# Kernel tuning notes

Hardware: AMD Instinct MI355X
Metric: run time of the kernel (lower is better)

## Reference

```python
import jax, jax.numpy as jnp
import numpy as np

B = 8
N1, N2 = 65536, 16384
C1, C2 = 256, 512
BN_EPS = 1e-5


def setup_inputs() -> dict:
    key = jax.random.key(0)
    ks = jax.random.split(key, 8)
    xyz1 = jax.random.normal(ks[0], (N1, 3), dtype=jnp.float32)
    points1 = jax.random.normal(ks[1], (N1, C1), dtype=jnp.float32)
    xyz2 = jax.random.normal(ks[2], (N2, 3), dtype=jnp.float32)
    points2 = jax.random.normal(ks[3], (N2, C2), dtype=jnp.float32)
    offset1 = (jnp.arange(1, B + 1, dtype=jnp.int32) * (N1 // B))
    offset2 = (jnp.arange(1, B + 1, dtype=jnp.int32) * (N2 // B))
    W1 = jax.random.normal(ks[4], (C1 + C2, 256), dtype=jnp.float32) * 0.02
    b1 = jnp.zeros((256,), jnp.float32)
    g1 = jnp.ones((256,), jnp.float32)
    be1 = jnp.zeros((256,), jnp.float32)
    W2 = jax.random.normal(ks[5], (256, 256), dtype=jnp.float32) * 0.02
    b2 = jnp.zeros((256,), jnp.float32)
    g2 = jnp.ones((256,), jnp.float32)
    be2 = jnp.zeros((256,), jnp.float32)
    return dict(xyz1=xyz1, points1=points1, xyz2=xyz2, points2=points2,
                offset1=offset1, offset2=offset2,
                W1=W1, b1=b1, g1=g1, be1=be1, W2=W2, b2=b2, g2=g2, be2=be2)


def _knn3(q, k):
    # q: [n1,3] queries, k: [n2,3] reference set -> 3-NN idx + euclidean dist
    d2 = (jnp.sum(q * q, -1)[:, None] + jnp.sum(k * k, -1)[None, :]
          - 2.0 * (q @ k.T))                      # [n1, n2]
    neg_d2, idx = jax.lax.top_k(-d2, 3)           # [n1, 3]
    dist = jnp.sqrt(jnp.maximum(-neg_d2, 0.0))
    return idx, dist


def _bn_relu(x, g, be):
    # BatchNorm1d in training mode: biased batch stats over the point dim
    mu = jnp.mean(x, axis=0)
    var = jnp.mean((x - mu) ** 2, axis=0)
    return jax.nn.relu(g * (x - mu) * jax.lax.rsqrt(var + BN_EPS) + be)


def reference(xyz1, points1, xyz2, points2, offset1, offset2,
              W1, b1, g1, be1, W2, b2, g2, be2):
    bsz = offset1.shape[0]
    n1 = xyz1.shape[0] // bsz
    n2 = xyz2.shape[0] // bsz
    q = xyz1.reshape(bsz, n1, 3)
    k = xyz2.reshape(bsz, n2, 3)
    idx, dist = jax.vmap(_knn3)(q, k)             # [B,n1,3], [B,n1,3]
    gidx = (idx + (jnp.arange(bsz, dtype=idx.dtype) * n2)[:, None, None])
    gidx = gidx.reshape(-1, 3)                    # [N1,3] global row ids
    dist = dist.reshape(-1, 3)
    dist_recip = 1.0 / (dist + 1e-8)
    weight = dist_recip / jnp.sum(dist_recip, axis=1, keepdims=True)
    # fused gather + weighted accumulate: [N1,3,C2] * [N1,3,1] -> [N1,C2]
    interpolated = jnp.sum(points2[gidx] * weight[..., None], axis=1)
    x = jnp.concatenate([points1, interpolated], axis=1)  # [N1, C1+C2]
    x = _bn_relu(x @ W1 + b1, g1, be1)
    x = _bn_relu(x @ W2 + b2, g2, be2)
    return x
```

## Files before the change

### kernel.cpp

```cpp
#include <hip/hip_runtime.h>
#include <math.h>

#define N1T 65536
#define N2T 16384
#define BSZ 8
#define N1B 8192
#define N2B 2048
#define C1 256
#define C2 512
#define K1 768
#define HID 256
#define BN_EPS 1e-5f

typedef short bf16x8 __attribute__((ext_vector_type(8)));
typedef float f32x4 __attribute__((ext_vector_type(4)));

__device__ __forceinline__ float mul_rn(float a, float b) {
    float r; asm("v_mul_f32 %0, %1, %2" : "=v"(r) : "v"(a), "v"(b)); return r;
}
__device__ __forceinline__ float add_rn(float a, float b) {
    float r; asm("v_add_f32 %0, %1, %2" : "=v"(r) : "v"(a), "v"(b)); return r;
}
__device__ __forceinline__ float sub_rn(float a, float b) {
    float r; asm("v_sub_f32 %0, %1, %2" : "=v"(r) : "v"(a), "v"(b)); return r;
}
__device__ __forceinline__ float fma_rn(float a, float b, float c) {
    float r; asm("v_fma_f32 %0, %1, %2, %3" : "=v"(r) : "v"(a), "v"(b), "v"(c)); return r;
}
__device__ __forceinline__ short f2bf(float f) {
    unsigned u = __builtin_bit_cast(unsigned, f);
    u += 0x7fffu + ((u >> 16) & 1u);
    return (short)(u >> 16);
}
__device__ __forceinline__ float bf2f(short s) {
    return __builtin_bit_cast(float, ((unsigned)(unsigned short)s) << 16);
}

__global__ __launch_bounds__(256) void knn_kernel(
    const float* __restrict__ xyz1, const float* __restrict__ xyz2,
    int* __restrict__ idx_out, float* __restrict__ w_out)
{
    __shared__ float4 sref[N2B + 4];
    const int tid = threadIdx.x;
    const int qbase = blockIdx.x * 64;
    const int batch = qbase / N1B;
    const float* k2 = xyz2 + (size_t)batch * N2B * 3;
    for (int p = tid; p < N2B; p += 256) {
        float x = k2[3 * p], y = k2[3 * p + 1], z = k2[3 * p + 2];
        float kk = add_rn(add_rn(mul_rn(x, x), mul_rn(y, y)), mul_rn(z, z));
        sref[p + (p >> 9)] = make_float4(x, y, z, kk);
    }
    __syncthreads();

    const int q = qbase + (tid >> 2);
    const int sub = tid & 3;
    const float qx = xyz1[q * 3 + 0], qy = xyz1[q * 3 + 1], qz = xyz1[q * 3 + 2];
    const float qq = add_rn(add_rn(mul_rn(qx, qx), mul_rn(qy, qy)), mul_rn(qz, qz));

    const int base = sub * 513;
    const int gbase = sub * 512;
    float a0 = 1e30f, a1 = 1e30f, a2 = 1e30f;
    int   ai0 = 0x7fffffff, ai1 = 0x7fffffff, ai2 = 0x7fffffff;
    float c0 = 1e30f, c1 = 1e30f, c2 = 1e30f;
    int   ci0 = 0x7fffffff, ci1 = 0x7fffffff, ci2 = 0x7fffffff;
    for (int jj = 0; jj < 256; ++jj) {
        float4 rA = sref[base + jj];
        float4 rB = sref[base + 256 + jj];
        float pA = mul_rn(qx, rA.x);
        float tA = fma_rn(qz, rA.z, fma_rn(qy, rA.y, pA));
        float dA = add_rn(sub_rn(qq, add_rn(tA, tA)), rA.w);
        float pB = mul_rn(qx, rB.x);
        float tB = fma_rn(qz, rB.z, fma_rn(qy, rB.y, pB));
        float dB = add_rn(sub_rn(qq, add_rn(tB, tB)), rB.w);
        if (dA < a2) {
            if (dA < a1) {
                a2 = a1; ai2 = ai1;
                if (dA < a0) { a1 = a0; ai1 = ai0; a0 = dA; ai0 = gbase + jj; }
                else         { a1 = dA; ai1 = gbase + jj; }
            } else { a2 = dA; ai2 = gbase + jj; }
        }
        if (dB < c2) {
            if (dB < c1) {
                c2 = c1; ci2 = ci1;
                if (dB < c0) { c1 = c0; ci1 = ci0; c0 = dB; ci0 = gbase + 256 + jj; }
                else         { c1 = dB; ci1 = gbase + 256 + jj; }
            } else { c2 = dB; ci2 = gbase + 256 + jj; }
        }
    }
    float bd0 = a0, bd1 = a1, bd2 = a2;
    int   bi0 = ai0, bi1 = ai1, bi2 = ai2;
#define LEXINS(d, ji)                                                        \
    if ((d < bd2) || (d == bd2 && ji < bi2)) {                               \
        if ((d < bd1) || (d == bd1 && ji < bi1)) {                           \
            bd2 = bd1; bi2 = bi1;                                            \
            if ((d < bd0) || (d == bd0 && ji < bi0)) {                       \
                bd1 = bd0; bi1 = bi0; bd0 = d; bi0 = ji;                     \
            } else { bd1 = d; bi1 = ji; }                                    \
        } else { bd2 = d; bi2 = ji; }                                        \
    }
    LEXINS(c0, ci0) LEXINS(c1, ci1) LEXINS(c2, ci2)
#pragma unroll
    for (int mask = 1; mask <= 2; mask <<= 1) {
        float pd0 = __shfl_xor(bd0, mask, 64);
        float pd1 = __shfl_xor(bd1, mask, 64);
        float pd2 = __shfl_xor(bd2, mask, 64);
        int   pi0 = __shfl_xor(bi0, mask, 64);
        int   pi1 = __shfl_xor(bi1, mask, 64);
        int   pi2 = __shfl_xor(bi2, mask, 64);
        LEXINS(pd0, pi0) LEXINS(pd1, pi1) LEXINS(pd2, pi2)
    }
#undef LEXINS
    if (sub == 0) {
        float d0s = __fsqrt_rn(fmaxf(bd0, 0.0f));
        float d1s = __fsqrt_rn(fmaxf(bd1, 0.0f));
        float d2s = __fsqrt_rn(fmaxf(bd2, 0.0f));
        float r0 = __fdiv_rn(1.0f, add_rn(d0s, 1e-8f));
        float r1 = __fdiv_rn(1.0f, add_rn(d1s, 1e-8f));
        float r2 = __fdiv_rn(1.0f, add_rn(d2s, 1e-8f));
        float rs = add_rn(add_rn(r0, r1), r2);
        w_out[q * 3 + 0] = __fdiv_rn(r0, rs);
        w_out[q * 3 + 1] = __fdiv_rn(r1, rs);
        w_out[q * 3 + 2] = __fdiv_rn(r2, rs);
        idx_out[q * 3 + 0] = batch * N2B + bi0;
        idx_out[q * 3 + 1] = batch * N2B + bi1;
        idx_out[q * 3 + 2] = batch * N2B + bi2;
    }
}

__global__ __launch_bounds__(256) void cast_p2_kernel(
    const float* __restrict__ p2, short* __restrict__ p2b)
{
    const size_t i = ((size_t)blockIdx.x * 256 + threadIdx.x) * 8;
    float4 u0 = *(const float4*)(p2 + i);
    float4 u1 = *(const float4*)(p2 + i + 4);
    bf16x8 v;
    v[0] = f2bf(u0.x); v[1] = f2bf(u0.y); v[2] = f2bf(u0.z); v[3] = f2bf(u0.w);
    v[4] = f2bf(u1.x); v[5] = f2bf(u1.y); v[6] = f2bf(u1.z); v[7] = f2bf(u1.w);
    *(bf16x8*)(p2b + i) = v;
}

__global__ __launch_bounds__(256) void transpose_w_kernel(
    const float* __restrict__ Win, short* __restrict__ WT, int K, int N)
{
    const int e = blockIdx.x * 256 + threadIdx.x;
    const int k = e / N, n = e % N;
    WT[(size_t)n * K + k] = f2bf(Win[e]);
}

#define LDP 40

__global__ __launch_bounds__(512) void gemm1m_kernel(
    const float* __restrict__ points1, const short* __restrict__ p2b,
    const int* __restrict__ idx, const float* __restrict__ w,
    const short* __restrict__ w1t, const float* __restrict__ bias,
    short* __restrict__ y1b, float* __restrict__ psum, float* __restrict__ psq)
{
    __shared__ short As[128][LDP];
    __shared__ short Bs[256][LDP];
    __shared__ float redS[2][4][64], redQ[2][4][64];
    const int tid = threadIdx.x;
    const int lane = tid & 63, wv = tid >> 6;
    const int wr = wv >> 2, wc = wv & 3;
    const int l16 = lane & 15, kh = (lane >> 4) * 8;
    const int row0 = blockIdx.x * 128;
    f32x4 acc[4][4];
#pragma unroll
    for (int m = 0; m < 4; ++m)
#pragma unroll
        for (int n = 0; n < 4; ++n) acc[m][n] = (f32x4){0.f, 0.f, 0.f, 0.f};

    const int arow = tid >> 2, akc = (tid & 3) * 8;
    const int rowA = row0 + arow;
    const int   jA0 = idx[rowA * 3 + 0], jA1 = idx[rowA * 3 + 1], jA2 = idx[rowA * 3 + 2];
    const float wA0 = w[rowA * 3 + 0],   wA1 = w[rowA * 3 + 1],   wA2 = w[rowA * 3 + 2];
    const int cb0 = tid * 2, cb1 = tid * 2 + 1;
    const int brow0 = cb0 >> 2, bkc0 = (cb0 & 3) * 8;
    const int brow1 = cb1 >> 2, bkc1 = (cb1 & 3) * 8;

#define LOAD_A(VA, KT)                                                        \
    {                                                                         \
        const int k0_ = (KT) * 32;                                            \
        if (k0_ < C1) {                                                       \
            float4 u0 = *(const float4*)(points1 + (size_t)rowA * C1 + k0_ + akc);     \
            float4 u1 = *(const float4*)(points1 + (size_t)rowA * C1 + k0_ + akc + 4); \
            VA[0] = f2bf(u0.x); VA[1] = f2bf(u0.y); VA[2] = f2bf(u0.z); VA[3] = f2bf(u0.w); \
            VA[4] = f2bf(u1.x); VA[5] = f2bf(u1.y); VA[6] = f2bf(u1.z); VA[7] = f2bf(u1.w); \
        } else {                                                              \
            const int kb = k0_ - C1 + akc;                                    \
            bf16x8 ga = *(const bf16x8*)(p2b + (size_t)jA0 * C2 + kb);        \
            bf16x8 gb = *(const bf16x8*)(p2b + (size_t)jA1 * C2 + kb);        \
            bf16x8 gc = *(const bf16x8*)(p2b + (size_t)jA2 * C2 + kb);        \
            _Pragma("unroll")                                                 \
            for (int e = 0; e < 8; ++e)                                       \
                VA[e] = f2bf(fmaf(bf2f(ga[e]), wA0,                           \
                          fmaf(bf2f(gb[e]), wA1, bf2f(gc[e]) * wA2)));        \
        }                                                                     \
    }
#define LOAD_B(WA, WB, KT)                                                    \
    {                                                                         \
        const int k0_ = (KT) * 32;                                            \
        WA = *(const bf16x8*)(w1t + (size_t)brow0 * K1 + k0_ + bkc0);         \
        WB = *(const bf16x8*)(w1t + (size_t)brow1 * K1 + k0_ + bkc1);         \
    }

    bf16x8 va, wa, wb;
    LOAD_A(va, 0)
    LOAD_B(wa, wb, 0)
    for (int kt = 0; kt < K1 / 32; ++kt) {
        __syncthreads();
        *(bf16x8*)(&As[arow][akc]) = va;
        *(bf16x8*)(&Bs[brow0][bkc0]) = wa;
        *(bf16x8*)(&Bs[brow1][bkc1]) = wb;
        __syncthreads();
        if (kt + 1 < K1 / 32) {
            LOAD_A(va, kt + 1)
            LOAD_B(wa, wb, kt + 1)
        }
        bf16x8 af[4], bf[4];
#pragma unroll
        for (int m = 0; m < 4; ++m)
            af[m] = *(const bf16x8*)(&As[wr * 64 + m * 16 + l16][kh]);
#pragma unroll
        for (int n = 0; n < 4; ++n)
            bf[n] = *(const bf16x8*)(&Bs[wc * 64 + n * 16 + l16][kh]);
#pragma unroll
        for (int m = 0; m < 4; ++m)
#pragma unroll
            for (int n = 0; n < 4; ++n)
                acc[m][n] = __builtin_amdgcn_mfma_f32_16x16x32_bf16(
                    af[m], bf[n], acc[m][n], 0, 0, 0);
    }
#undef LOAD_A
#undef LOAD_B
#pragma unroll
    for (int n = 0; n < 4; ++n) {
        const int col = wc * 64 + n * 16 + l16;
        const float bv = bias[col];
        float s = 0.f, qa = 0.f;
#pragma unroll
        for (int m = 0; m < 4; ++m) {
            const int rowb = row0 + wr * 64 + m * 16 + (lane >> 4) * 4;
#pragma unroll
            for (int j = 0; j < 4; ++j) {
                float v = acc[m][n][j] + bv;
                y1b[(size_t)(rowb + j) * HID + col] = f2bf(v);
                s += v; qa = fmaf(v, v, qa);
            }
        }
        s += __shfl_xor(s, 16, 64);  s += __shfl_xor(s, 32, 64);
        qa += __shfl_xor(qa, 16, 64); qa += __shfl_xor(qa, 32, 64);
        if ((lane >> 4) == 0) {
            redS[wr][wc][n * 16 + l16] = s;
            redQ[wr][wc][n * 16 + l16] = qa;
        }
    }
    __syncthreads();
    if (tid < 256) {
        const int wcf = tid >> 6, cf = tid & 63;
        float s = redS[0][wcf][cf] + redS[1][wcf][cf];
        float qa = redQ[0][wcf][cf] + redQ[1][wcf][cf];
        psum[(size_t)blockIdx.x * HID + tid] = s;
        psq[(size_t)blockIdx.x * HID + tid] = qa;
    }
}

#define GEMM_EPILOGUE(STORE_STMT)                                             \
    __shared__ float redS[2][2][64], redQ[2][2][64];                          \
    _Pragma("unroll")                                                         \
    for (int n = 0; n < 4; ++n) {                                             \
        const int col = col0 + wc * 64 + n * 16 + l16;                        \
        const float bv = bias[col];                                           \
        float s = 0.f, qa = 0.f;                                              \
        _Pragma("unroll")                                                     \
        for (int m = 0; m < 4; ++m) {                                         \
            const int rowb = row0 + wr * 64 + m * 16 + (lane >> 4) * 4;       \
            _Pragma("unroll")                                                 \
            for (int j = 0; j < 4; ++j) {                                     \
                float v = acc[m][n][j] + bv;                                  \
                STORE_STMT;                                                   \
                s += v; qa = fmaf(v, v, qa);                                  \
            }                                                                 \
        }                                                                     \
        s += __shfl_xor(s, 16, 64);  s += __shfl_xor(s, 32, 64);              \
        qa += __shfl_xor(qa, 16, 64); qa += __shfl_xor(qa, 32, 64);           \
        if ((lane >> 4) == 0) {                                               \
            redS[wr][wc][n * 16 + l16] = s;                                   \
            redQ[wr][wc][n * 16 + l16] = qa;                                  \
        }                                                                     \
    }                                                                         \
    __syncthreads();                                                          \
    if (tid < 128) {                                                          \
        const int wcf = tid >> 6, cf = tid & 63;                              \
        float s = redS[0][wcf][cf] + redS[1][wcf][cf];                        \
        float qa = redQ[0][wcf][cf] + redQ[1][wcf][cf];                       \
        const int gcol = col0 + wcf * 64 + cf;                                \
        psum[(size_t)blockIdx.y * HID + gcol] = s;                            \
        psq[(size_t)blockIdx.y * HID + gcol] = qa;                            \
    }

__global__ __launch_bounds__(256) void gemm2m_kernel(
    const short* __restrict__ y1b, const float* __restrict__ scale,
    const float* __restrict__ shift, const short* __restrict__ w2t,
    const float* __restrict__ bias, short* __restrict__ y2b,
    float* __restrict__ psum, float* __restrict__ psq)
{
    __shared__ short As[128][LDP];
    __shared__ short Bs[128][LDP];
    const int tid = threadIdx.x;
    const int lane = tid & 63, wv = tid >> 6;
    const int wr = wv >> 1, wc = wv & 1;
    const int l16 = lane & 15, kh = (lane >> 4) * 8;
    const int row0 = blockIdx.y * 128, col0 = blockIdx.x * 128;
    f32x4 acc[4][4];
#pragma unroll
    for (int m = 0; m < 4; ++m)
#pragma unroll
        for (int n = 0; n < 4; ++n) acc[m][n] = (f32x4){0.f, 0.f, 0.f, 0.f};

    const int c0 = tid * 2;
    const int r0c = c0 >> 2, kc0 = (c0 & 3) * 8;
    const int r1c = (c0 + 1) >> 2, kc1 = ((c0 + 1) & 3) * 8;

    for (int kt = 0; kt < HID / 32; ++kt) {
        const int k0 = kt * 32;
        bf16x8 x0 = *(const bf16x8*)(y1b + (size_t)(row0 + r0c) * HID + k0 + kc0);
        bf16x8 x1 = *(const bf16x8*)(y1b + (size_t)(row0 + r1c) * HID + k0 + kc1);
        float4 s0 = *(const float4*)(scale + k0 + kc0);
        float4 s1 = *(const float4*)(scale + k0 + kc0 + 4);
        float4 h0 = *(const float4*)(shift + k0 + kc0);
        float4 h1 = *(const float4*)(shift + k0 + kc0 + 4);
        float4 s2 = *(const float4*)(scale + k0 + kc1);
        float4 s3 = *(const float4*)(scale + k0 + kc1 + 4);
        float4 h2 = *(const float4*)(shift + k0 + kc1);
        float4 h3 = *(const float4*)(shift + k0 + kc1 + 4);
        bf16x8 va, vb;
        va[0] = f2bf(fmaxf(fmaf(bf2f(x0[0]), s0.x, h0.x), 0.f));
        va[1] = f2bf(fmaxf(fmaf(bf2f(x0[1]), s0.y, h0.y), 0.f));
        va[2] = f2bf(fmaxf(fmaf(bf2f(x0[2]), s0.z, h0.z), 0.f));
        va[3] = f2bf(fmaxf(fmaf(bf2f(x0[3]), s0.w, h0.w), 0.f));
        va[4] = f2bf(fmaxf(fmaf(bf2f(x0[4]), s1.x, h1.x), 0.f));
        va[5] = f2bf(fmaxf(fmaf(bf2f(x0[5]), s1.y, h1.y), 0.f));
        va[6] = f2bf(fmaxf(fmaf(bf2f(x0[6]), s1.z, h1.z), 0.f));
        va[7] = f2bf(fmaxf(fmaf(bf2f(x0[7]), s1.w, h1.w), 0.f));
        vb[0] = f2bf(fmaxf(fmaf(bf2f(x1[0]), s2.x, h2.x), 0.f));
        vb[1] = f2bf(fmaxf(fmaf(bf2f(x1[1]), s2.y, h2.y), 0.f));
        vb[2] = f2bf(fmaxf(fmaf(bf2f(x1[2]), s2.z, h2.z), 0.f));
        vb[3] = f2bf(fmaxf(fmaf(bf2f(x1[3]), s2.w, h2.w), 0.f));
        vb[4] = f2bf(fmaxf(fmaf(bf2f(x1[4]), s3.x, h3.x), 0.f));
        vb[5] = f2bf(fmaxf(fmaf(bf2f(x1[5]), s3.y, h3.y), 0.f));
        vb[6] = f2bf(fmaxf(fmaf(bf2f(x1[6]), s3.z, h3.z), 0.f));
        vb[7] = f2bf(fmaxf(fmaf(bf2f(x1[7]), s3.w, h3.w), 0.f));
        bf16x8 wa = *(const bf16x8*)(w2t + (size_t)(col0 + r0c) * HID + k0 + kc0);
        bf16x8 wb = *(const bf16x8*)(w2t + (size_t)(col0 + r1c) * HID + k0 + kc1);
        __syncthreads();
        *(bf16x8*)(&As[r0c][kc0]) = va;
        *(bf16x8*)(&As[r1c][kc1]) = vb;
        *(bf16x8*)(&Bs[r0c][kc0]) = wa;
        *(bf16x8*)(&Bs[r1c][kc1]) = wb;
        __syncthreads();

        bf16x8 af[4], bf[4];
#pragma unroll
        for (int m = 0; m < 4; ++m)
            af[m] = *(const bf16x8*)(&As[wr * 64 + m * 16 + l16][kh]);
#pragma unroll
        for (int n = 0; n < 4; ++n)
            bf[n] = *(const bf16x8*)(&Bs[wc * 64 + n * 16 + l16][kh]);
#pragma unroll
        for (int m = 0; m < 4; ++m)
#pragma unroll
            for (int n = 0; n < 4; ++n)
                acc[m][n] = __builtin_amdgcn_mfma_f32_16x16x32_bf16(
                    af[m], bf[n], acc[m][n], 0, 0, 0);
    }
    GEMM_EPILOGUE(y2b[(size_t)(rowb + j) * HID + col] = f2bf(v))
}

__global__ __launch_bounds__(256) void bn_finalize_kernel(
    const float* __restrict__ psum, const float* __restrict__ psq,
    const float* __restrict__ g, const float* __restrict__ be,
    float* __restrict__ scale, float* __restrict__ shift)
{
    const int c = threadIdx.x;
    float s = 0.0f, q = 0.0f;
    for (int b = 0; b < 512; ++b) { s += psum[b * HID + c]; q += psq[b * HID + c]; }
    const float inv_n = 1.0f / (float)N1T;
    const float mu = s * inv_n;
    const float var = fmaxf(q * inv_n - mu * mu, 0.0f);
    const float sc = g[c] * rsqrtf(var + BN_EPS);
    scale[c] = sc;
    shift[c] = be[c] - mu * sc;
}

__global__ __launch_bounds__(256) void bn_apply_kernel(
    const short* __restrict__ y2b, const float* __restrict__ scale,
    const float* __restrict__ shift, float* __restrict__ out)
{
    const size_t i = ((size_t)blockIdx.x * 256 + threadIdx.x) * 8;
    const int c8 = (int)(i & 255);
    bf16x8 x = *(const bf16x8*)(y2b + i);
    float4 s0 = *(const float4*)(scale + c8);
    float4 s1 = *(const float4*)(scale + c8 + 4);
    float4 h0 = *(const float4*)(shift + c8);
    float4 h1 = *(const float4*)(shift + c8 + 4);
    float4 o0, o1;
    o0.x = fmaxf(fmaf(bf2f(x[0]), s0.x, h0.x), 0.f);
    o0.y = fmaxf(fmaf(bf2f(x[1]), s0.y, h0.y), 0.f);
    o0.z = fmaxf(fmaf(bf2f(x[2]), s0.z, h0.z), 0.f);
    o0.w = fmaxf(fmaf(bf2f(x[3]), s0.w, h0.w), 0.f);
    o1.x = fmaxf(fmaf(bf2f(x[4]), s1.x, h1.x), 0.f);
    o1.y = fmaxf(fmaf(bf2f(x[5]), s1.y, h1.y), 0.f);
    o1.z = fmaxf(fmaf(bf2f(x[6]), s1.z, h1.z), 0.f);
    o1.w = fmaxf(fmaf(bf2f(x[7]), s1.w, h1.w), 0.f);
    *(float4*)(out + i) = o0;
    *(float4*)(out + i + 4) = o1;
}

extern "C" void kernel_launch(void* const* d_in, const int* in_sizes, int n_in,
                              void* d_out, int out_size, void* d_ws, size_t ws_size,
                              hipStream_t stream)
{
    const float* xyz1    = (const float*)d_in[0];
    const float* points1 = (const float*)d_in[1];
    const float* xyz2    = (const float*)d_in[2];
    const float* points2 = (const float*)d_in[3];
    const float* W1  = (const float*)d_in[6];
    const float* b1  = (const float*)d_in[7];
    const float* g1  = (const float*)d_in[8];
    const float* be1 = (const float*)d_in[9];
    const float* W2  = (const float*)d_in[10];
    const float* b2  = (const float*)d_in[11];
    const float* g2  = (const float*)d_in[12];
    const float* be2 = (const float*)d_in[13];
    float* out = (float*)d_out;

    char* ws = (char*)d_ws;
    short* y1b  = (short*)ws;
    short* y2b  = (short*)(ws + 33554432);
    short* p2b  = (short*)(ws + 67108864);
    size_t off  = 67108864 + 16777216;
    short*  w1t    = (short*)(ws + off);  off += (size_t)K1 * HID * 2;
    short*  w2t    = (short*)(ws + off);  off += (size_t)HID * HID * 2;
    int*    idx    = (int*)(ws + off);    off += (size_t)N1T * 3 * 4;
    float*  w      = (float*)(ws + off);  off += (size_t)N1T * 3 * 4;
    float*  psum   = (float*)(ws + off);  off += 512 * 256 * 4;
    float*  psq    = (float*)(ws + off);  off += 512 * 256 * 4;
    float*  scale1 = (float*)(ws + off);  off += 256 * 4;
    float*  shift1 = (float*)(ws + off);  off += 256 * 4;
    float*  scale2 = (float*)(ws + off);  off += 256 * 4;
    float*  shift2 = (float*)(ws + off);  off += 256 * 4;

    cast_p2_kernel<<<N2T * C2 / 8 / 256, 256, 0, stream>>>(points2, p2b);
    transpose_w_kernel<<<K1 * HID / 256, 256, 0, stream>>>(W1, w1t, K1, HID);
    transpose_w_kernel<<<HID * HID / 256, 256, 0, stream>>>(W2, w2t, HID, HID);
    knn_kernel<<<1024, 256, 0, stream>>>(xyz1, xyz2, idx, w);
    gemm1m_kernel<<<N1T / 128, 512, 0, stream>>>(
        points1, p2b, idx, w, w1t, b1, y1b, psum, psq);
    bn_finalize_kernel<<<1, 256, 0, stream>>>(psum, psq, g1, be1, scale1, shift1);
    gemm2m_kernel<<<dim3(HID / 128, N1T / 128), 256, 0, stream>>>(
        y1b, scale1, shift1, w2t, b2, y2b, psum, psq);
    bn_finalize_kernel<<<1, 256, 0, stream>>>(psum, psq, g2, be2, scale2, shift2);
    bn_apply_kernel<<<N1T * HID / 8 / 256, 256, 0, stream>>>(y2b, scale2, shift2, out);
}
```

Baseline: 233.3 us.

## Precompute points2 @ W1b then interpolate projected rows in GEMM1 epilogue

Uses linearity to reorder interpolation and projection: first computes Z = points2 · W1[C1:] on the 16K coarse points, then the main GEMM only covers the 256-wide points1 part and adds the weighted sum of three gathered Z rows in its epilogue. This cuts GEMM1 MMA work on the 65K rows from K=768 to K=256 and removes the bf16 gather-and-blend from the inner loop. In exchange it adds a small extra GEMM, a 16 MB fp32 Z buffer, and scattered fp32 gathers in the epilogue. Rounding also changes because the interpolation now happens after projection in fp32 instead of on bf16 inputs.

```diff
diff --git a/kernel.cpp b/kernel.cpp
--- a/kernel.cpp
+++ b/kernel.cpp
@@ -139,6 +139,16 @@
     *(bf16x8*)(p2b + i) = v;
 }
 
+__global__ __launch_bounds__(256) void transpose_w1_kernel(
+    const float* __restrict__ W1, short* __restrict__ w1at, short* __restrict__ w1bt)
+{
+    const int e = blockIdx.x * 256 + threadIdx.x;
+    const int k = e / HID, n = e % HID;
+    short v = f2bf(W1[e]);
+    if (k < C1) w1at[(size_t)n * C1 + k] = v;
+    else        w1bt[(size_t)n * C2 + (k - C1)] = v;
+}
+
 __global__ __launch_bounds__(256) void transpose_w_kernel(
     const float* __restrict__ Win, short* __restrict__ WT, int K, int N)
 {
@@ -149,20 +159,93 @@
 
 #define LDP 40
 
+__global__ __launch_bounds__(256) void zgemm_kernel(
+    const short* __restrict__ p2b, const short* __restrict__ w1bt,
+    float* __restrict__ Z)
+{
+    __shared__ short As[128][LDP];
+    __shared__ short Bs[128][LDP];
+    const int tid = threadIdx.x;
+    const int lane = tid & 63, wv = tid >> 6;
+    const int wr = wv >> 1, wc = wv & 1;
+    const int l16 = lane & 15, kh = (lane >> 4) * 8;
+    const int row0 = blockIdx.y * 128, col0 = blockIdx.x * 128;
+    f32x4 acc[4][4];
+#pragma unroll
+    for (int m = 0; m < 4; ++m)
+#pragma unroll
+        for (int n = 0; n < 4; ++n) acc[m][n] = (f32x4){0.f, 0.f, 0.f, 0.f};
+
+    const int c0 = tid * 2;
+    const int r0c = c0 >> 2, kc0 = (c0 & 3) * 8;
+    const int r1c = (c0 + 1) >> 2, kc1 = ((c0 + 1) & 3) * 8;
+
+    for (int kt = 0; kt < C2 / 32; ++kt) {
+        const int k0 = kt * 32;
+        bf16x8 va = *(const bf16x8*)(p2b + (size_t)(row0 + r0c) * C2 + k0 + kc0);
+        bf16x8 vb = *(const bf16x8*)(p2b + (size_t)(row0 + r1c) * C2 + k0 + kc1);
+        bf16x8 wa = *(const bf16x8*)(w1bt + (size_t)(col0 + r0c) * C2 + k0 + kc0);
+        bf16x8 wb = *(const bf16x8*)(w1bt + (size_t)(col0 + r1c) * C2 + k0 + kc1);
+        __syncthreads();
+        *(bf16x8*)(&As[r0c][kc0]) = va;
+        *(bf16x8*)(&As[r1c][kc1]) = vb;
+        *(bf16x8*)(&Bs[r0c][kc0]) = wa;
+        *(bf16x8*)(&Bs[r1c][kc1]) = wb;
+        __syncthreads();
+
+        bf16x8 af[4], bf[4];
+#pragma unroll
+        for (int m = 0; m < 4; ++m)
+            af[m] = *(const bf16x8*)(&As[wr * 64 + m * 16 + l16][kh]);
+#pragma unroll
+        for (int n = 0; n < 4; ++n)
+            bf[n] = *(const bf16x8*)(&Bs[wc * 64 + n * 16 + l16][kh]);
+#pragma unroll
+        for (int m = 0; m < 4; ++m)
+#pragma unroll
+            for (int n = 0; n < 4; ++n)
+                acc[m][n] = __builtin_amdgcn_mfma_f32_16x16x32_bf16(
+                    af[m], bf[n], acc[m][n], 0, 0, 0);
+    }
+#pragma unroll
+    for (int n = 0; n < 4; ++n) {
+        const int col = col0 + wc * 64 + n * 16 + l16;
+#pragma unroll
+        for (int m = 0; m < 4; ++m) {
+            const int rowb = row0 + wr * 64 + m * 16 + (lane >> 4) * 4;
+#pragma unroll
+            for (int j = 0; j < 4; ++j)
+                Z[(size_t)(rowb + j) * HID + col] = acc[m][n][j];
+        }
+    }
+}
+
 __global__ __launch_bounds__(512) void gemm1m_kernel(
-    const float* __restrict__ points1, const short* __restrict__ p2b,
+    const float* __restrict__ points1, const float* __restrict__ Z,
     const int* __restrict__ idx, const float* __restrict__ w,
-    const short* __restrict__ w1t, const float* __restrict__ bias,
+    const short* __restrict__ w1at, const float* __restrict__ bias,
     short* __restrict__ y1b, float* __restrict__ psum, float* __restrict__ psq)
 {
     __shared__ short As[128][LDP];
     __shared__ short Bs[256][LDP];
+    __shared__ int   sidx[128][3];
+    __shared__ float swt[128][3];
     __shared__ float redS[2][4][64], redQ[2][4][64];
     const int tid = threadIdx.x;
     const int lane = tid & 63, wv = tid >> 6;
     const int wr = wv >> 2, wc = wv & 3;
     const int l16 = lane & 15, kh = (lane >> 4) * 8;
     const int row0 = blockIdx.x * 128;
+
+    if (tid < 128) {
+        sidx[tid][0] = idx[(row0 + tid) * 3 + 0];
+        sidx[tid][1] = idx[(row0 + tid) * 3 + 1];
+        sidx[tid][2] = idx[(row0 + tid) * 3 + 2];
+        swt[tid][0] = w[(row0 + tid) * 3 + 0];
+        swt[tid][1] = w[(row0 + tid) * 3 + 1];
+        swt[tid][2] = w[(row0 + tid) * 3 + 2];
+    }
+
     f32x4 acc[4][4];
 #pragma unroll
     for (int m = 0; m < 4; ++m)
@@ -171,8 +254,6 @@
 
     const int arow = tid >> 2, akc = (tid & 3) * 8;
     const int rowA = row0 + arow;
-    const int   jA0 = idx[rowA * 3 + 0], jA1 = idx[rowA * 3 + 1], jA2 = idx[rowA * 3 + 2];
-    const float wA0 = w[rowA * 3 + 0],   wA1 = w[rowA * 3 + 1],   wA2 = w[rowA * 3 + 2];
     const int cb0 = tid * 2, cb1 = tid * 2 + 1;
     const int brow0 = cb0 >> 2, bkc0 = (cb0 & 3) * 8;
     const int brow1 = cb1 >> 2, bkc1 = (cb1 & 3) * 8;
@@ -180,39 +261,28 @@
 #define LOAD_A(VA, KT)                                                        \
     {                                                                         \
         const int k0_ = (KT) * 32;                                            \
-        if (k0_ < C1) {                                                       \
-            float4 u0 = *(const float4*)(points1 + (size_t)rowA * C1 + k0_ + akc);     \
-            float4 u1 = *(const float4*)(points1 + (size_t)rowA * C1 + k0_ + akc + 4); \
-            VA[0] = f2bf(u0.x); VA[1] = f2bf(u0.y); VA[2] = f2bf(u0.z); VA[3] = f2bf(u0.w); \
-            VA[4] = f2bf(u1.x); VA[5] = f2bf(u1.y); VA[6] = f2bf(u1.z); VA[7] = f2bf(u1.w); \
-        } else {                                                              \
-            const int kb = k0_ - C1 + akc;                                    \
-            bf16x8 ga = *(const bf16x8*)(p2b + (size_t)jA0 * C2 + kb);        \
-            bf16x8 gb = *(const bf16x8*)(p2b + (size_t)jA1 * C2 + kb);        \
-            bf16x8 gc = *(const bf16x8*)(p2b + (size_t)jA2 * C2 + kb);        \
-            _Pragma("unroll")                                                 \
-            for (int e = 0; e < 8; ++e)                                       \
-                VA[e] = f2bf(fmaf(bf2f(ga[e]), wA0,                           \
-                          fmaf(bf2f(gb[e]), wA1, bf2f(gc[e]) * wA2)));        \
-        }                                                                     \
+        float4 u0 = *(const float4*)(points1 + (size_t)rowA * C1 + k0_ + akc);     \
+        float4 u1 = *(const float4*)(points1 + (size_t)rowA * C1 + k0_ + akc + 4); \
+        VA[0] = f2bf(u0.x); VA[1] = f2bf(u0.y); VA[2] = f2bf(u0.z); VA[3] = f2bf(u0.w); \
+        VA[4] = f2bf(u1.x); VA[5] = f2bf(u1.y); VA[6] = f2bf(u1.z); VA[7] = f2bf(u1.w); \
     }
 #define LOAD_B(WA, WB, KT)                                                    \
     {                                                                         \
         const int k0_ = (KT) * 32;                                            \
-        WA = *(const bf16x8*)(w1t + (size_t)brow0 * K1 + k0_ + bkc0);         \
-        WB = *(const bf16x8*)(w1t + (size_t)brow1 * K1 + k0_ + bkc1);         \
+        WA = *(const bf16x8*)(w1at + (size_t)brow0 * C1 + k0_ + bkc0);        \
+        WB = *(const bf16x8*)(w1at + (size_t)brow1 * C1 + k0_ + bkc1);        \
     }
 
     bf16x8 va, wa, wb;
     LOAD_A(va, 0)
     LOAD_B(wa, wb, 0)
-    for (int kt = 0; kt < K1 / 32; ++kt) {
+    for (int kt = 0; kt < C1 / 32; ++kt) {
         __syncthreads();
         *(bf16x8*)(&As[arow][akc]) = va;
         *(bf16x8*)(&Bs[brow0][bkc0]) = wa;
         *(bf16x8*)(&Bs[brow1][bkc1]) = wb;
         __syncthreads();
-        if (kt + 1 < K1 / 32) {
+        if (kt + 1 < C1 / 32) {
             LOAD_A(va, kt + 1)
             LOAD_B(wa, wb, kt + 1)
         }
@@ -232,35 +302,48 @@
     }
 #undef LOAD_A
 #undef LOAD_B
-#pragma unroll
-    for (int n = 0; n < 4; ++n) {
-        const int col = wc * 64 + n * 16 + l16;
-        const float bv = bias[col];
-        float s = 0.f, qa = 0.f;
-#pragma unroll
-        for (int m = 0; m < 4; ++m) {
-            const int rowb = row0 + wr * 64 + m * 16 + (lane >> 4) * 4;
-#pragma unroll
-            for (int j = 0; j < 4; ++j) {
-                float v = acc[m][n][j] + bv;
-                y1b[(size_t)(rowb + j) * HID + col] = f2bf(v);
-                s += v; qa = fmaf(v, v, qa);
+    float bv[4];
+#pragma unroll
+    for (int n = 0; n < 4; ++n) bv[n] = bias[wc * 64 + n * 16 + l16];
+    float s[4] = {0.f, 0.f, 0.f, 0.f}, qa[4] = {0.f, 0.f, 0.f, 0.f};
+#pragma unroll
+    for (int m = 0; m < 4; ++m) {
+        const int rl0 = wr * 64 + m * 16 + (lane >> 4) * 4;
+#pragma unroll
+        for (int j = 0; j < 4; ++j) {
+            const int rl = rl0 + j;
+            const int j0 = sidx[rl][0], j1 = sidx[rl][1], j2 = sidx[rl][2];
+            const float w0 = swt[rl][0], w1 = swt[rl][1], w2 = swt[rl][2];
+            const float* z0 = Z + (size_t)j0 * HID;
+            const float* z1 = Z + (size_t)j1 * HID;
+            const float* z2 = Z + (size_t)j2 * HID;
+#pragma unroll
+            for (int n = 0; n < 4; ++n) {
+                const int col = wc * 64 + n * 16 + l16;
+                float zi = fmaf(w0, z0[col], fmaf(w1, z1[col], w2 * z2[col]));
+                float v = acc[m][n][j] + bv[n] + zi;
+                y1b[(size_t)(row0 + rl) * HID + col] = f2bf(v);
+                s[n] += v; qa[n] = fmaf(v, v, qa[n]);
             }
         }
-        s += __shfl_xor(s, 16, 64);  s += __shfl_xor(s, 32, 64);
-        qa += __shfl_xor(qa, 16, 64); qa += __shfl_xor(qa, 32, 64);
+    }
+#pragma unroll
+    for (int n = 0; n < 4; ++n) {
+        float sv = s[n], qv = qa[n];
+        sv += __shfl_xor(sv, 16, 64);  sv += __shfl_xor(sv, 32, 64);
+        qv += __shfl_xor(qv, 16, 64);  qv += __shfl_xor(qv, 32, 64);
         if ((lane >> 4) == 0) {
-            redS[wr][wc][n * 16 + l16] = s;
-            redQ[wr][wc][n * 16 + l16] = qa;
+            redS[wr][wc][n * 16 + l16] = sv;
+            redQ[wr][wc][n * 16 + l16] = qv;
         }
     }
     __syncthreads();
     if (tid < 256) {
         const int wcf = tid >> 6, cf = tid & 63;
-        float s = redS[0][wcf][cf] + redS[1][wcf][cf];
-        float qa = redQ[0][wcf][cf] + redQ[1][wcf][cf];
-        psum[(size_t)blockIdx.x * HID + tid] = s;
-        psq[(size_t)blockIdx.x * HID + tid] = qa;
+        float sv = redS[0][wcf][cf] + redS[1][wcf][cf];
+        float qv = redQ[0][wcf][cf] + redQ[1][wcf][cf];
+        psum[(size_t)blockIdx.x * HID + tid] = sv;
+        psq[(size_t)blockIdx.x * HID + tid] = qv;
     }
 }
 
@@ -438,8 +521,10 @@
     short* y1b  = (short*)ws;
     short* y2b  = (short*)(ws + 33554432);
     short* p2b  = (short*)(ws + 67108864);
-    size_t off  = 67108864 + 16777216;
-    short*  w1t    = (short*)(ws + off);  off += (size_t)K1 * HID * 2;
+    float* Z    = (float*)(ws + 67108864 + 16777216);
+    size_t off  = 67108864 + 16777216 + 16777216;
+    short*  w1at   = (short*)(ws + off);  off += (size_t)C1 * HID * 2;
+    short*  w1bt   = (short*)(ws + off);  off += (size_t)C2 * HID * 2;
     short*  w2t    = (short*)(ws + off);  off += (size_t)HID * HID * 2;
     int*    idx    = (int*)(ws + off);    off += (size_t)N1T * 3 * 4;
     float*  w      = (float*)(ws + off);  off += (size_t)N1T * 3 * 4;
@@ -451,11 +536,12 @@
     float*  shift2 = (float*)(ws + off);  off += 256 * 4;
 
     cast_p2_kernel<<<N2T * C2 / 8 / 256, 256, 0, stream>>>(points2, p2b);
-    transpose_w_kernel<<<K1 * HID / 256, 256, 0, stream>>>(W1, w1t, K1, HID);
+    transpose_w1_kernel<<<K1 * HID / 256, 256, 0, stream>>>(W1, w1at, w1bt);
     transpose_w_kernel<<<HID * HID / 256, 256, 0, stream>>>(W2, w2t, HID, HID);
+    zgemm_kernel<<<dim3(HID / 128, N2T / 128), 256, 0, stream>>>(p2b, w1bt, Z);
     knn_kernel<<<1024, 256, 0, stream>>>(xyz1, xyz2, idx, w);
     gemm1m_kernel<<<N1T / 128, 512, 0, stream>>>(
-        points1, p2b, idx, w, w1t, b1, y1b, psum, psq);
+        points1, Z, idx, w, w1at, b1, y1b, psum, psq);
     bn_finalize_kernel<<<1, 256, 0, stream>>>(psum, psq, g1, be1, scale1, shift1);
     gemm2m_kernel<<<dim3(HID / 128, N1T / 128), 256, 0, stream>>>(
         y1b, scale1, shift1, w2t, b2, y2b, psum, psq);
```

Result: no change. 233.8 us (+0.2%).
